# Kernel optimization log

Hardware: AMD Instinct MI355X
Metric: run time of the kernel (lower is better)

## Reference

```python
import jax, jax.numpy as jnp
import numpy as np
import math

B, S, D, NH = 2, 2048, 1024, 16
DK = D // NH
E, TOPK, MOE_H, NSH = 8, 2, 1024, 2
SH_H = MOE_H * NSH
EPS = 1e-6


def setup_inputs() -> dict:
    key = jax.random.key(0)
    ks = jax.random.split(key, 24)
    p = lambda k, shape: jax.random.normal(k, shape, jnp.float32) * 0.02
    x = jax.random.normal(ks[0], (B, S, D), jnp.float32)
    # RoPE tables: freqs_cis = exp(i * t * theta^{-2j/dk}), passed as cos/sin
    inv = 1.0 / (10000.0 ** (np.arange(0, DK, 2, dtype=np.float32) / DK))
    ang = np.outer(np.arange(S, dtype=np.float32), inv)
    freqs_cos = jnp.asarray(np.cos(ang), jnp.float32)
    freqs_sin = jnp.asarray(np.sin(ang), jnp.float32)
    mask = jnp.triu(jnp.full((S, S), -1e9, jnp.float32), k=1)  # causal additive mask
    return {
        'x': x, 'freqs_cos': freqs_cos, 'freqs_sin': freqs_sin, 'mask': mask,
        'wq': p(ks[1], (D, D)), 'wk': p(ks[2], (D, D)),
        'wv': p(ks[3], (D, D)), 'wo': p(ks[4], (D, D)),
        'attn_norm_w': jnp.ones((D,), jnp.float32),
        'ffn_norm_w': jnp.ones((D,), jnp.float32),
        'gate_w': p(ks[5], (E, D)), 'gate_b': p(ks[6], (E,)),
        'w1': p(ks[7], (E, MOE_H, D)), 'b1': p(ks[8], (E, MOE_H)),
        'w2': p(ks[9], (E, D, MOE_H)), 'b2': p(ks[10], (E, D)),
        'w3': p(ks[11], (E, MOE_H, D)), 'b3': p(ks[12], (E, MOE_H)),
        'sg_w': p(ks[13], (SH_H, D)), 'su_w': p(ks[14], (SH_H, D)),
        'sd_w': p(ks[15], (D, SH_H)),
    }


def rmsnorm(x, w):
    f = x.astype(jnp.float32)
    y = f * jax.lax.rsqrt(jnp.mean(f * f, axis=-1, keepdims=True) + EPS)
    return y.astype(x.dtype) * w


def rope(t, cos, sin):
    # t: [b, s, h, dk]; pairs (t[2j], t[2j+1]) as complex, multiplied by e^{i ang}
    tr, ti = t[..., 0::2], t[..., 1::2]
    c, s = cos[None, :, None, :], sin[None, :, None, :]
    outr = tr * c - ti * s
    outi = tr * s + ti * c
    return jnp.stack([outr, outi], axis=-1).reshape(t.shape)


def reference(x, freqs_cos, freqs_sin, mask, wq, wk, wv, wo, attn_norm_w, ffn_norm_w,
              gate_w, gate_b, w1, b1, w2, b2, w3, b3, sg_w, su_w, sd_w):
    b, s, d = x.shape
    # --- attention with RoPE ---
    h = rmsnorm(x, attn_norm_w)
    q = (h @ wq.T).reshape(b, s, NH, DK)
    k = (h @ wk.T).reshape(b, s, NH, DK)
    v = (h @ wv.T).reshape(b, s, NH, DK)
    q = rope(q, freqs_cos, freqs_sin)
    k = rope(k, freqs_cos, freqs_sin)
    scale = 1.0 / math.sqrt(DK)
    q = q.transpose(0, 2, 1, 3)
    k = k.transpose(0, 2, 1, 3)
    v = v.transpose(0, 2, 1, 3)
    scores = jnp.einsum('bhqd,bhkd->bhqk', q, k) * scale + mask
    # NOTE: source divides by sqrt(d_k) a second time before softmax (faithful quirk)
    attn = jax.nn.softmax(scores * scale, axis=-1)
    o = jnp.einsum('bhqk,bhkd->bhqd', attn, v).transpose(0, 2, 1, 3).reshape(b, s, d)
    x = x + o @ wo.T
    # --- MoE FFN ---
    hf = rmsnorm(x, ffn_norm_w).reshape(-1, d)                 # [T, D]
    gscores = jax.nn.softmax(hf @ gate_w.T + gate_b, axis=-1)  # [T, E]
    _, idx = jax.lax.top_k(gscores, TOPK)                      # bias is None -> topk on scores
    weights = jnp.take_along_axis(gscores, idx, axis=1)        # original_scores gather
    wmask = (jax.nn.one_hot(idx, E, dtype=hf.dtype) * weights[..., None]).sum(1)  # [T, E]
    shared = (jax.nn.silu(hf @ sg_w.T) * (hf @ su_w.T)) @ sd_w.T
    a1 = jnp.einsum('td,ehd->teh', hf, w1) + b1
    a3 = jnp.einsum('td,ehd->teh', hf, w3) + b3
    eo = jnp.einsum('teh,edh->ted', jax.nn.silu(a1) * a3, w2) + b2  # [T, E, D]
    router = jnp.einsum('te,ted->td', wmask, eo)
    return x + (shared + router).reshape(x.shape)
```

## Files before the change

### kernel.cpp

```cpp
#include <hip/hip_runtime.h>


typedef unsigned short u16;
typedef __attribute__((ext_vector_type(8))) short bh8;
typedef __attribute__((ext_vector_type(4))) float fv4;
typedef __attribute__((ext_vector_type(4))) unsigned uv4;
typedef __attribute__((ext_vector_type(2))) int iv2;

#define LOG2E 1.4426950408889634f
#define MAX_TILES 71

__device__ __forceinline__ float b2f(u16 u) {
  return __builtin_bit_cast(float, ((unsigned)u) << 16);
}
__device__ __forceinline__ u16 f2b(float f) {
  unsigned x = __builtin_bit_cast(unsigned, f);
  return (u16)((x + 0x7fffu + ((x >> 16) & 1u)) >> 16);
}
__device__ __forceinline__ fv4 mfma16(bh8 a, bh8 b, fv4 c) {
  return __builtin_amdgcn_mfma_f32_16x16x32_bf16(a, b, c, 0, 0, 0);
}
__device__ __forceinline__ unsigned cvtpk(float lo, float hi) {
  unsigned r;
  asm("v_cvt_pk_bf16_f32 %0, %1, %2" : "=v"(r) : "v"(lo), "v"(hi));
  return r;
}

__device__ __forceinline__ void xcd_swizzle(int& bx, int& by) {
  int gx = gridDim.x;
  int nwg = gx * gridDim.y;
  int flat = by * gx + bx;
  int q = nwg >> 3, r = nwg & 7;
  int xcd = flat & 7, idx = flat >> 3;
  int swz = (xcd < r ? xcd * (q + 1) : r * (q + 1) + (xcd - r) * q) + idx;
  by = swz / gx;
  bx = swz - by * gx;
}

#define GLD16(g, l)                                                        \
  __builtin_amdgcn_global_load_lds(                                        \
      (const __attribute__((address_space(1))) void*)(g),                  \
      (__attribute__((address_space(3))) void*)(l), 16, 0, 0)

__device__ __forceinline__ bh8 lds_frag(const u16* base, int row, int b8) {
  int off = row * 128 + ((b8 * 16) ^ ((row & 7) << 4));
  return *(const bh8*)((const char*)base + off);
}

template <int MODE, int TM = 128>
__global__ __launch_bounds__(256) void gemm_bt(
    const u16* __restrict__ A, const u16* __restrict__ B, int M, int N, int K,
    u16* __restrict__ Cb, float* __restrict__ Cf,
    const float* __restrict__ add1, const float* __restrict__ add2,
    const float* __restrict__ bias, const int* __restrict__ tmeta,
    const int* __restrict__ etok) {
  constexpr int MR = TM / 32;
  __shared__ u16 As[2][TM * 64];
  __shared__ u16 Bs[2][128 * 64];
  int bx = blockIdx.x, by = blockIdx.y;
  xcd_swizzle(bx, by);
  const int lane = threadIdx.x & 63;
  const int wid = threadIdx.x >> 6;
  const int wr = wid >> 1, wc = wid & 1;
  const int n0 = bx * 128;
  const int rr = lane >> 3;
  const int b8s = (lane & 7) ^ rr;
  const int ldA = (MODE == 6) ? M : K;

  int m0 = 0, e = 0, m0l = 0, cnt = 0, row0 = 0;
  const u16* Bp = B;
  if constexpr (MODE == 6 || MODE == 8) {
    int tile = by;
    if (tile >= tmeta[0]) return;
    e = tmeta[16 + tile * 4];
    m0l = tmeta[17 + tile * 4];
    cnt = tmeta[18 + tile * 4];
    row0 = tmeta[19 + tile * 4];
    Bp = B + (size_t)e * N * K;
  } else {
    m0 = by * TM;
  }

  const u16* Arow[MR];
  const u16* Brow[4];
#pragma unroll
  for (int i = 0; i < MR; ++i) {
    int c = wid * MR + i;
    int row = c * 8 + rr;
    if constexpr (MODE == 8) {
      int li = m0l + row;
      li = li < cnt ? li : cnt - 1;
      int tok = etok[e * 4096 + li];
      Arow[i] = A + (size_t)tok * ldA + b8s * 8;
    } else if constexpr (MODE == 6) {
      Arow[i] = A + (size_t)(row0 + row) * ldA + b8s * 8;
    } else {
      Arow[i] = A + (size_t)(m0 + row) * ldA + b8s * 8;
    }
  }
#pragma unroll
  for (int i = 0; i < 4; ++i)
    Brow[i] = Bp + (size_t)(n0 + (wid * 4 + i) * 8 + rr) * K + b8s * 8;

  fv4 acc[MR][4] = {};
  const int nt = K >> 6;

#pragma unroll
  for (int i = 0; i < MR; ++i)
    GLD16(Arow[i], &As[0][(wid * MR + i) * 512]);
#pragma unroll
  for (int i = 0; i < 4; ++i)
    GLD16(Brow[i], &Bs[0][(wid * 4 + i) * 512]);

  for (int t = 0; t < nt; ++t) {
    const int cur = t & 1;
    if (t + 1 < nt) {
      const int k0 = (t + 1) * 64;
#pragma unroll
      for (int i = 0; i < MR; ++i)
        GLD16(Arow[i] + k0, &As[cur ^ 1][(wid * MR + i) * 512]);
#pragma unroll
      for (int i = 0; i < 4; ++i)
        GLD16(Brow[i] + k0, &Bs[cur ^ 1][(wid * 4 + i) * 512]);
      if constexpr (MR == 4)
        asm volatile("s_waitcnt vmcnt(8)" ::: "memory");
      else
        asm volatile("s_waitcnt vmcnt(6)" ::: "memory");
    } else {
      asm volatile("s_waitcnt vmcnt(0)" ::: "memory");
    }
    __builtin_amdgcn_s_barrier();
    __builtin_amdgcn_sched_barrier(0);

#pragma unroll
    for (int ks = 0; ks < 2; ++ks) {
      int b8 = ks * 4 + (lane >> 4);
      bh8 af[MR], bf[4];
#pragma unroll
      for (int mi = 0; mi < MR; ++mi)
        af[mi] = lds_frag(As[cur], wr * (16 * MR) + mi * 16 + (lane & 15), b8);
#pragma unroll
      for (int ni = 0; ni < 4; ++ni)
        bf[ni] = lds_frag(Bs[cur], wc * 64 + ni * 16 + (lane & 15), b8);
      __builtin_amdgcn_s_setprio(1);
#pragma unroll
      for (int mi = 0; mi < MR; ++mi)
#pragma unroll
        for (int ni = 0; ni < 4; ++ni)
          acc[mi][ni] = mfma16(af[mi], bf[ni], acc[mi][ni]);
      __builtin_amdgcn_s_setprio(0);
    }
    __builtin_amdgcn_sched_barrier(0);
    __builtin_amdgcn_s_barrier();
    __builtin_amdgcn_sched_barrier(0);
  }

  const int rbase = (MODE == 6 || MODE == 8) ? row0 : m0;
  const int r0b = rbase + wr * (16 * MR) + (lane >> 4) * 4;
  const int c0b = n0 + wc * 64 + (lane & 15);

  if constexpr (MODE == 7 || MODE == 8) {
    const int OUTN = N >> 1;
    const int colb = (n0 >> 1) + wc * 32;
    const float* bb1 = nullptr;
    const float* bb3 = nullptr;
    if constexpr (MODE == 8) {
      bb1 = add1 + (size_t)e * OUTN;
      bb3 = add2 + (size_t)e * OUTN;
    }
#pragma unroll
    for (int mi = 0; mi < MR; ++mi) {
#pragma unroll
      for (int ni = 0; ni < 2; ++ni) {
        int c = colb + ni * 16 + (lane & 15);
#pragma unroll
        for (int r = 0; r < 4; ++r) {
          int row = r0b + mi * 16 + r;
          float xg = acc[mi][ni][r];
          float yu = acc[mi][ni + 2][r];
          if constexpr (MODE == 8) {
            xg += bb1[c];
            yu += bb3[c];
          }
          float s = xg / (1.f + __expf(-xg));
          Cb[(size_t)row * OUTN + c] = f2b(s * yu);
        }
      }
    }
  } else if constexpr (MODE == 9) {
#pragma unroll
    for (int mi = 0; mi < MR; ++mi) {
#pragma unroll
      for (int r = 0; r < 4; ++r) {
        int row = r0b + mi * 16 + r;
        int g0 = tmeta[2 * row], g1 = tmeta[2 * row + 1];
        float w0 = bias[2 * row], w1 = bias[2 * row + 1];
        const u16* e0p = Cb + (size_t)g0 * 1024;
        const u16* e1p = Cb + (size_t)g1 * 1024;
#pragma unroll
        for (int ni = 0; ni < 4; ++ni) {
          int c = c0b + ni * 16;
          size_t idx = (size_t)row * N + c;
          Cf[idx] = add1[idx] + acc[mi][ni][r] + w0 * b2f(e0p[c]) +
                    w1 * b2f(e1p[c]);
        }
      }
    }
  } else {
    const float* bb = nullptr;
    if constexpr (MODE == 6) bb = bias + (size_t)e * N;
#pragma unroll
    for (int mi = 0; mi < MR; ++mi) {
#pragma unroll
      for (int ni = 0; ni < 4; ++ni) {
        int c = c0b + ni * 16;
#pragma unroll
        for (int r = 0; r < 4; ++r) {
          int row = r0b + mi * 16 + r;
          size_t idx = (size_t)row * N + c;
          float v = acc[mi][ni][r];
          if constexpr (MODE == 0) Cb[idx] = f2b(v);
          else if constexpr (MODE == 1) Cf[idx] = add1[idx] + v;
          else Cb[idx] = f2b(v + bb[c]);
        }
      }
    }
  }
}

__global__ __launch_bounds__(256) void rmsnorm_bf16(
    const float* __restrict__ x, const float* __restrict__ w,
    u16* __restrict__ out) {
  int t = blockIdx.x;
  const float* xr = x + (size_t)t * 1024;
  fv4 v = *(const fv4*)(xr + threadIdx.x * 4);
  float ss = v[0] * v[0] + v[1] * v[1] + v[2] * v[2] + v[3] * v[3];
#pragma unroll
  for (int off = 1; off < 64; off <<= 1) ss += __shfl_xor(ss, off);
  __shared__ float red[4];
  int lane = threadIdx.x & 63, wid = threadIdx.x >> 6;
  if (lane == 0) red[wid] = ss;
  __syncthreads();
  float inv = rsqrtf((red[0] + red[1] + red[2] + red[3]) * (1.0f / 1024.f) + 1e-6f);
  u16* op = out + (size_t)t * 1024 + threadIdx.x * 4;
  const float* wp = w + threadIdx.x * 4;
#pragma unroll
  for (int i = 0; i < 4; ++i) op[i] = f2b(v[i] * inv * wp[i]);
}

__global__ __launch_bounds__(256) void rope_repack(
    const u16* __restrict__ qkv, const float* __restrict__ fc,
    const float* __restrict__ fs, u16* __restrict__ qr, u16* __restrict__ kr,
    u16* __restrict__ vt, int S) {
  __shared__ u16 tile[64][65];
  const int s0 = blockIdx.x * 64;
  const int b = blockIdx.y;
  const int h0 = blockIdx.z * 4;
#pragma unroll 4
  for (int it = 0; it < 32; ++it) {
    int idx = threadIdx.x + it * 256;
    int tl = idx >> 7, rem = idx & 127;
    int h = h0 + (rem >> 5), i = rem & 31;
    int s = s0 + tl;
    float c = fc[s * 32 + i], sn = fs[s * 32 + i];
    size_t src = ((size_t)(b * S + s)) * 3072 + h * 64 + 2 * i;
    size_t dst = ((size_t)((b * 16 + h) * S + s)) * 64 + 2 * i;
    float a0 = b2f(qkv[src]), a1 = b2f(qkv[src + 1]);
    qr[dst] = f2b(a0 * c - a1 * sn);
    qr[dst + 1] = f2b(a0 * sn + a1 * c);
    float b0 = b2f(qkv[src + 1024]), b1 = b2f(qkv[src + 1025]);
    kr[dst] = f2b(b0 * c - b1 * sn);
    kr[dst + 1] = f2b(b0 * sn + b1 * c);
  }
  for (int hh = 0; hh < 4; ++hh) {
    int h = h0 + hh;
    __syncthreads();
    for (int cc = threadIdx.x; cc < 512; cc += 256) {
      int tl = cc >> 3, d8 = cc & 7;
      bh8 val = *(const bh8*)(qkv + ((size_t)(b * S + s0 + tl)) * 3072 + 2048 +
                              h * 64 + d8 * 8);
#pragma unroll
      for (int j = 0; j < 8; ++j) tile[tl][d8 * 8 + j] = (u16)val[j];
    }
    __syncthreads();
    for (int cc = threadIdx.x; cc < 512; cc += 256) {
      int d = cc >> 3, pg = cc & 7;
      int sbase = 16 * (pg >> 2) + 4 * (pg & 3);
      bh8 o;
#pragma unroll
      for (int j = 0; j < 8; ++j)
        o[j] = (short)tile[sbase + (j & 3) + ((j >> 2) << 5)][d];
      *(bh8*)(vt + ((size_t)((b * 16 + h) * 64 + d)) * S + s0 + pg * 8) = o;
    }
  }
}

__global__ __launch_bounds__(256) void attn_fwd(
    const u16* __restrict__ qr, const u16* __restrict__ kr,
    const u16* __restrict__ vt, u16* __restrict__ ob, int S, int NHc) {
  __shared__ u16 Ks[2][64 * 64];
  __shared__ u16 Vs[2][64 * 64];
  const int lane = threadIdx.x & 63;
  const int wid = threadIdx.x >> 6;
  const int g = lane >> 4;
  const int l15 = lane & 15;
  const int bh = blockIdx.x;
  const int ia = blockIdx.y;
  const int nq = S / 64;
  const int qa0 = ia * 64;
  const int qb0 = (nq - 1 - ia) * 64;
  const int b = bh / NHc, h = bh % NHc;
  const u16* qbase = qr + (size_t)bh * S * 64;
  const u16* kb = kr + (size_t)bh * S * 64;
  const u16* vb = vt + (size_t)bh * 64 * S;
  const float SC = 0.015625f * LOG2E;
  const int rr = lane >> 3;
  const int b8s = (lane & 7) ^ rr;

  bh8 ONES;
#pragma unroll
  for (int j = 0; j < 8; ++j) ONES[j] = (short)0x3f80;

  bh8 qfA[2], qfB[2];
  {
    const u16* qp = qbase + (size_t)(qa0 + wid * 16 + l15) * 64 + g * 8;
    qfA[0] = *(const bh8*)qp;
    qfA[1] = *(const bh8*)(qp + 32);
    qp = qbase + (size_t)(qb0 + wid * 16 + l15) * 64 + g * 8;
    qfB[0] = *(const bh8*)qp;
    qfB[1] = *(const bh8*)(qp + 32);
  }
  fv4 oaccA[4] = {}, oaccB[4] = {};
  fv4 lA = {}, lB = {};
  float mA = -1e30f, mB = -1e30f;
  const int nktB = nq - ia;

  auto stage = [&](int buf, int j0) {
#pragma unroll
    for (int i = 0; i < 2; ++i) {
      int c = wid * 2 + i;
      int row = c * 8 + rr;
      GLD16(kb + (size_t)(j0 + row) * 64 + b8s * 8, &Ks[buf][c * 512]);
      GLD16(vb + (size_t)row * S + j0 + b8s * 8, &Vs[buf][c * 512]);
    }
  };
  stage(0, 0);

  auto process = [&](const bh8 (&kf)[2][4], const bh8 (&vf)[2][4], int j0,
                     int q0x, bh8* qf, fv4* oacc, float& mrow, fv4& lrowC) {
    const int q_my = q0x + wid * 16 + l15;
    fv4 st[4] = {};
    __builtin_amdgcn_s_setprio(1);
#pragma unroll
    for (int ks = 0; ks < 2; ++ks)
#pragma unroll
      for (int jt = 0; jt < 4; ++jt)
        st[jt] = mfma16(kf[ks][jt], qf[ks], st[jt]);
    __builtin_amdgcn_s_setprio(0);

    float sr[4][4];
    float mloc = -1e30f;
    const int jb = j0 + 4 * g;
    if (j0 + 63 > q0x + wid * 16) {
#pragma unroll
      for (int jt = 0; jt < 4; ++jt)
#pragma unroll
        for (int r = 0; r < 4; ++r) {
          int j = jb + jt * 16 + r;
          float s = (j <= q_my) ? st[jt][r] : -1e30f;
          sr[jt][r] = s;
          mloc = fmaxf(mloc, s);
        }
    } else {
#pragma unroll
      for (int jt = 0; jt < 4; ++jt)
#pragma unroll
        for (int r = 0; r < 4; ++r) {
          sr[jt][r] = st[jt][r];
          mloc = fmaxf(mloc, st[jt][r]);
        }
    }
    mloc = fmaxf(mloc, __shfl_xor(mloc, 16));
    mloc = fmaxf(mloc, __shfl_xor(mloc, 32));
    mloc *= SC;
    bool defer = __all(mloc <= mrow + 8.f);
    if (!defer) {
      float mnew = fmaxf(mrow, mloc);
      float sfac = exp2f(mrow - mnew);
      mrow = mnew;
      float sfC[4];
#pragma unroll
      for (int r = 0; r < 4; ++r) sfC[r] = __shfl(sfac, g * 4 + r);
#pragma unroll
      for (int dt = 0; dt < 4; ++dt)
#pragma unroll
        for (int r = 0; r < 4; ++r) oacc[dt][r] *= sfC[r];
#pragma unroll
      for (int r = 0; r < 4; ++r) lrowC[r] *= sfC[r];
    }
    float p[4][4];
#pragma unroll
    for (int jt = 0; jt < 4; ++jt)
#pragma unroll
      for (int r = 0; r < 4; ++r)
        p[jt][r] = exp2f(fmaf(sr[jt][r], SC, -mrow));

    __builtin_amdgcn_s_setprio(1);
    fv4 racc = {};
#pragma unroll
    for (int ks = 0; ks < 2; ++ks) {
      uv4 w;
      w[0] = cvtpk(p[ks][0], p[ks][1]);
      w[1] = cvtpk(p[ks][2], p[ks][3]);
      w[2] = cvtpk(p[ks + 2][0], p[ks + 2][1]);
      w[3] = cvtpk(p[ks + 2][2], p[ks + 2][3]);
      bh8 pa = __builtin_bit_cast(bh8, w);
      racc = mfma16(pa, ONES, racc);
#pragma unroll
      for (int dt = 0; dt < 4; ++dt)
        oacc[dt] = mfma16(pa, vf[ks][dt], oacc[dt]);
    }
    __builtin_amdgcn_s_setprio(0);
#pragma unroll
    for (int r = 0; r < 4; ++r) lrowC[r] += racc[r];
  };

  for (int kt = 0; kt < nktB; ++kt) {
    const int j0 = kt * 64;
    __syncthreads();
    if (kt + 1 < nktB) stage((kt + 1) & 1, (kt + 1) * 64);
    const u16* Kc = Ks[kt & 1];
    const u16* Vc = Vs[kt & 1];
    bh8 kf[2][4], vf[2][4];
#pragma unroll
    for (int ks = 0; ks < 2; ++ks) {
      int b8 = ks * 4 + g;
#pragma unroll
      for (int jt = 0; jt < 4; ++jt)
        kf[ks][jt] = lds_frag(Kc, jt * 16 + l15, b8);
#pragma unroll
      for (int dt = 0; dt < 4; ++dt)
        vf[ks][dt] = lds_frag(Vc, dt * 16 + l15, b8);
    }
    process(kf, vf, j0, qb0, qfB, oaccB, mB, lB);
    if (kt <= ia) process(kf, vf, j0, qa0, qfA, oaccA, mA, lA);
  }

  auto wout = [&](fv4* oacc, fv4 lrowC, int q0x) {
#pragma unroll
    for (int dt = 0; dt < 4; ++dt)
#pragma unroll
      for (int r = 0; r < 4; ++r) {
        int row = q0x + wid * 16 + g * 4 + r;
        int col = dt * 16 + l15;
        ob[((size_t)b * S + row) * 1024 + h * 64 + col] =
            f2b(oacc[dt][r] / lrowC[r]);
      }
  };
  wout(oaccA, lA, qa0);
  wout(oaccB, lB, qb0);
}

__global__ __launch_bounds__(256) void gate_topk(
    const float* __restrict__ x2, const float* __restrict__ nw,
    const float* __restrict__ gw, const float* __restrict__ gb,
    int* __restrict__ topk_e, float* __restrict__ topk_w,
    u16* __restrict__ hf) {
  int t = blockIdx.x * 4 + (threadIdx.x >> 6);
  int lane = threadIdx.x & 63;
  const float* xr = x2 + (size_t)t * 1024;
  float hv[16];
  float ss = 0.f;
#pragma unroll
  for (int i = 0; i < 4; ++i) {
    fv4 v = *(const fv4*)(xr + lane * 16 + i * 4);
#pragma unroll
    for (int j = 0; j < 4; ++j) {
      hv[i * 4 + j] = v[j];
      ss += v[j] * v[j];
    }
  }
#pragma unroll
  for (int off = 1; off < 64; off <<= 1) ss += __shfl_xor(ss, off);
  float inv = rsqrtf(ss * (1.0f / 1024.f) + 1e-6f);
  const fv4* nwp = (const fv4*)(nw + lane * 16);
#pragma unroll
  for (int i = 0; i < 4; ++i) {
    fv4 wv = nwp[i];
#pragma unroll
    for (int j = 0; j < 4; ++j) hv[i * 4 + j] *= inv * wv[j];
  }
  {
    bh8 o0, o1;
#pragma unroll
    for (int j = 0; j < 8; ++j) {
      o0[j] = (short)f2b(hv[j]);
      o1[j] = (short)f2b(hv[8 + j]);
    }
    u16* hp = hf + (size_t)t * 1024 + lane * 16;
    *(bh8*)hp = o0;
    *(bh8*)(hp + 8) = o1;
  }
  float logit[8];
#pragma unroll
  for (int e = 0; e < 8; ++e) {
    const fv4* wp = (const fv4*)(gw + (size_t)e * 1024 + lane * 16);
    float s = 0.f;
#pragma unroll
    for (int i = 0; i < 4; ++i) {
      fv4 wv = wp[i];
#pragma unroll
      for (int j = 0; j < 4; ++j) s += hv[i * 4 + j] * wv[j];
    }
    logit[e] = s;
  }
#pragma unroll
  for (int off = 1; off < 64; off <<= 1)
#pragma unroll
    for (int e = 0; e < 8; ++e) logit[e] += __shfl_xor(logit[e], off);
  if (lane == 0) {
#pragma unroll
    for (int e = 0; e < 8; ++e) logit[e] += gb[e];
    float mx = logit[0];
#pragma unroll
    for (int e = 1; e < 8; ++e) mx = fmaxf(mx, logit[e]);
    float pe[8], se = 0.f;
#pragma unroll
    for (int e = 0; e < 8; ++e) { pe[e] = __expf(logit[e] - mx); se += pe[e]; }
    float rs = 1.f / se;
#pragma unroll
    for (int e = 0; e < 8; ++e) pe[e] *= rs;
    int i0 = 0;
    float b0 = pe[0];
#pragma unroll
    for (int e = 1; e < 8; ++e)
      if (pe[e] > b0) { b0 = pe[e]; i0 = e; }
    int i1 = -1;
    float b1v = -1.f;
#pragma unroll
    for (int e = 0; e < 8; ++e)
      if (e != i0 && pe[e] > b1v) { b1v = pe[e]; i1 = e; }
    topk_e[2 * t] = i0;
    topk_e[2 * t + 1] = i1;
    topk_w[2 * t] = b0;
    topk_w[2 * t + 1] = b1v;
  }
}

__global__ __launch_bounds__(512) void route_tokens(
    const int* __restrict__ topk_e, int* __restrict__ pos_of,
    int* __restrict__ etok, int* __restrict__ meta, int* __restrict__ rowid,
    int T2) {
  __shared__ int scnt[8], sbase[8];
  const int e = threadIdx.x >> 6;
  const int lane = threadIdx.x & 63;
  int base = 0;
  for (int i0 = 0; i0 < T2; i0 += 128) {
    iv2 te = *(const iv2*)(topk_e + i0 + lane * 2);
    unsigned long long m0 = __ballot(te[0] == e);
    unsigned long long m1 = __ballot(te[1] == e);
    unsigned long long lt = (1ull << lane) - 1;
    int pre = __popcll(m0 & lt) + __popcll(m1 & lt);
    if (te[0] == e) {
      int pos = base + pre;
      etok[e * 4096 + pos] = (i0 >> 1) + lane;
      pos_of[i0 + lane * 2] = pos;
      ++pre;
    }
    if (te[1] == e) {
      int pos = base + pre;
      etok[e * 4096 + pos] = (i0 >> 1) + lane;
      pos_of[i0 + lane * 2 + 1] = pos;
    }
    base += __popcll(m0) + __popcll(m1);
  }
  if (lane == 0) scnt[e] = base;
  __syncthreads();
  if (threadIdx.x == 0) {
    int tt = 0, rb = 0;
#pragma unroll
    for (int e2 = 0; e2 < 8; ++e2) {
      sbase[e2] = rb;
      int c = scnt[e2];
      int nt = (c + 127) >> 7;
      for (int i = 0; i < nt; ++i) {
        meta[16 + tt * 4] = e2;
        meta[17 + tt * 4] = i * 128;
        meta[18 + tt * 4] = c;
        meta[19 + tt * 4] = rb + i * 128;
        ++tt;
      }
      rb += nt * 128;
    }
    meta[0] = tt;
  }
  __syncthreads();
  for (int i = threadIdx.x; i < T2; i += 512)
    rowid[i] = sbase[topk_e[i]] + pos_of[i];
}

__global__ __launch_bounds__(256) void f2b_convert(
    const float* __restrict__ src, u16* __restrict__ dst) {
  size_t i = ((size_t)blockIdx.x * 256 + threadIdx.x) * 8;
  fv4 a = *(const fv4*)(src + i);
  fv4 b = *(const fv4*)(src + i + 4);
  bh8 o;
#pragma unroll
  for (int j = 0; j < 4; ++j) o[j] = (short)f2b(a[j]);
#pragma unroll
  for (int j = 0; j < 4; ++j) o[4 + j] = (short)f2b(b[j]);
  *(bh8*)(dst + i) = o;
}

__global__ __launch_bounds__(256) void f2b_convert_ilv(
    const float* __restrict__ src, u16* __restrict__ dst, int half,
    int seg_shift) {
  size_t i = ((size_t)blockIdx.x * 256 + threadIdx.x) * 8;
  int r = (int)(i >> 10), col = (int)(i & 1023);
  int rl = r & ((1 << seg_shift) - 1), e = r >> seg_shift;
  int dstrow = (e << (seg_shift + 1)) + ((rl >> 5) << 6) + (rl & 31) +
               (half << 5);
  fv4 a = *(const fv4*)(src + i);
  fv4 b = *(const fv4*)(src + i + 4);
  bh8 o;
#pragma unroll
  for (int j = 0; j < 4; ++j) o[j] = (short)f2b(a[j]);
#pragma unroll
  for (int j = 0; j < 4; ++j) o[4 + j] = (short)f2b(b[j]);
  *(bh8*)(dst + (size_t)dstrow * 1024 + col) = o;
}

extern "C" void kernel_launch(void* const* d_in, const int* in_sizes, int n_in,
                              void* d_out, int out_size, void* d_ws,
                              size_t ws_size, hipStream_t stream) {
  (void)in_sizes; (void)n_in; (void)out_size; (void)ws_size;
  const int Sc = 2048, Dc = 1024, NHc = 16, Tc = 4096, SH = 2048;

  const float* x   = (const float*)d_in[0];
  const float* fc  = (const float*)d_in[1];
  const float* fs  = (const float*)d_in[2];
  const float* wq  = (const float*)d_in[4];
  const float* wk  = (const float*)d_in[5];
  const float* wv  = (const float*)d_in[6];
  const float* wo  = (const float*)d_in[7];
  const float* anw = (const float*)d_in[8];
  const float* fnw = (const float*)d_in[9];
  const float* gw  = (const float*)d_in[10];
  const float* gb  = (const float*)d_in[11];
  const float* w1  = (const float*)d_in[12];
  const float* b1  = (const float*)d_in[13];
  const float* w2  = (const float*)d_in[14];
  const float* b2  = (const float*)d_in[15];
  const float* w3  = (const float*)d_in[16];
  const float* b3  = (const float*)d_in[17];
  const float* sgw = (const float*)d_in[18];
  const float* suw = (const float*)d_in[19];
  const float* sdw = (const float*)d_in[20];
  float* out = (float*)d_out;

  char* base = (char*)d_ws;
  size_t off = 0;
  auto alloc = [&](size_t bytes) -> void* {
    void* p = base + off;
    off += (bytes + 255) & ~(size_t)255;
    return p;
  };
  u16* wqkv_b = (u16*)alloc(2ull * 3072 * 1024);
  u16* wo_b   = (u16*)alloc(2ull * 1024 * 1024);
  u16* sgu_b  = (u16*)alloc(2ull * 4096 * 1024);
  u16* sdw_b  = (u16*)alloc(2ull * 1024 * 2048);
  u16* w13_b  = (u16*)alloc(2ull * 8 * 2048 * 1024);
  u16* w2_b   = (u16*)alloc(2ull * 8 * 1024 * 1024);
  char* regA = (char*)alloc(2ull * Tc * 4096);
  char* regB = (char*)alloc(2ull * (size_t)MAX_TILES * 128 * 2048);
  float* x2  = (float*)alloc(4ull * Tc * Dc);
  u16* hs_b  = (u16*)alloc(2ull * Tc * SH);
  int* topk_e = (int*)alloc(2ull * Tc * 4);
  float* topk_w = (float*)alloc(2ull * Tc * 4);
  int* pos_of = (int*)alloc(2ull * Tc * 4);
  int* rowid = (int*)alloc(2ull * Tc * 4);
  int* etok = (int*)alloc(8ull * 4096 * 4);
  int* meta = (int*)alloc(512 * 4);

  u16* qkv_out = (u16*)regA;
  u16* eo_c    = (u16*)regA;
  u16* h_b  = (u16*)regB;
  u16* qr   = (u16*)regB;
  u16* kr   = (u16*)(regB + 2ull * Tc * Dc);
  u16* vt_  = (u16*)(regB + 4ull * Tc * Dc);
  u16* o_b  = (u16*)(regB + 6ull * Tc * Dc);
  u16* a13_c = (u16*)regB;
  u16* hf_b = wqkv_b;

  auto conv = [&](const float* s, u16* d, size_t n) {
    f2b_convert<<<dim3((unsigned)(n / 2048)), 256, 0, stream>>>(s, d);
  };
  conv(wq, wqkv_b, (size_t)Dc * Dc);
  conv(wk, wqkv_b + 1048576, (size_t)Dc * Dc);
  conv(wv, wqkv_b + 2097152, (size_t)Dc * Dc);
  conv(wo, wo_b, (size_t)Dc * Dc);
  conv(sdw, sdw_b, (size_t)Dc * SH);
  conv(w2, w2_b, 8ull * 1024 * 1024);
  f2b_convert_ilv<<<1024, 256, 0, stream>>>(sgw, sgu_b, 0, 11);
  f2b_convert_ilv<<<1024, 256, 0, stream>>>(suw, sgu_b, 1, 11);
  f2b_convert_ilv<<<4096, 256, 0, stream>>>(w1, w13_b, 0, 10);
  f2b_convert_ilv<<<4096, 256, 0, stream>>>(w3, w13_b, 1, 10);

  rmsnorm_bf16<<<Tc, 256, 0, stream>>>(x, anw, h_b);
  gemm_bt<0><<<dim3(3072 / 128, Tc / 128), 256, 0, stream>>>(
      h_b, wqkv_b, Tc, 3072, Dc, qkv_out, nullptr, nullptr, nullptr, nullptr,
      nullptr, nullptr);
  rope_repack<<<dim3(Sc / 64, 2, 4), 256, 0, stream>>>(qkv_out, fc, fs, qr, kr,
                                                       vt_, Sc);
  attn_fwd<<<dim3(2 * NHc, Sc / 128), 256, 0, stream>>>(qr, kr, vt_, o_b, Sc,
                                                        NHc);
  gemm_bt<1, 64><<<dim3(Dc / 128, Tc / 64), 256, 0, stream>>>(
      o_b, wo_b, Tc, Dc, Dc, nullptr, x2, x, nullptr, nullptr, nullptr,
      nullptr);

  gate_topk<<<Tc / 4, 256, 0, stream>>>(x2, fnw, gw, gb, topk_e, topk_w,
                                        hf_b);
  route_tokens<<<1, 512, 0, stream>>>(topk_e, pos_of, etok, meta, rowid,
                                      2 * Tc);

  gemm_bt<7><<<dim3(4096 / 128, Tc / 128), 256, 0, stream>>>(
      hf_b, sgu_b, Tc, 4096, Dc, hs_b, nullptr, nullptr, nullptr, nullptr,
      nullptr, nullptr);

  gemm_bt<8><<<dim3(2048 / 128, MAX_TILES), 256, 0, stream>>>(
      hf_b, w13_b, Tc, 2048, Dc, a13_c, nullptr, b1, b3, nullptr, meta, etok);
  gemm_bt<6><<<dim3(Dc / 128, MAX_TILES), 256, 0, stream>>>(
      a13_c, w2_b, 1024, Dc, 1024, eo_c, nullptr, nullptr, nullptr,
      b2, meta, etok);

  gemm_bt<9, 64><<<dim3(Dc / 128, Tc / 64), 256, 0, stream>>>(
      hs_b, sdw_b, Tc, Dc, SH, eo_c, out, x2, nullptr, topk_w, rowid,
      nullptr);
}
```

Baseline: 406.6 us.

## Use 4-stage BK=32 LDS pipeline in gemm_bt instead of double-buffered BK=64

Restructures the GEMM main loop from a two-buffer pipeline with 64-wide K tiles into a four-buffer ring with 32-wide K tiles. Loads run three stages ahead, with waitcnt values graded for the tail. It adds a new 32-column LDS swizzle (lds_frag32) and remaps global-to-LDS loads to match. The goal is to hide global load latency behind more in-flight stages at the same LDS footprint. The cost is twice as many barriers per unit of K and fewer MFMAs between barriers.

Result: slower. 446.4 us (+9.8%).

```diff
diff --git a/kernel.cpp b/kernel.cpp
--- a/kernel.cpp
+++ b/kernel.cpp
@@ -42,6 +42,11 @@
       (const __attribute__((address_space(1))) void*)(g),                  \
       (__attribute__((address_space(3))) void*)(l), 16, 0, 0)
 
+__device__ __forceinline__ bh8 lds_frag32(const u16* base, int row, int g) {
+  int off = (row << 5) + (((g ^ (row >> 1)) & 3) << 3);
+  return *(const bh8*)(base + off);
+}
+
 __device__ __forceinline__ bh8 lds_frag(const u16* base, int row, int b8) {
   int off = row * 128 + ((b8 * 16) ^ ((row & 7) << 4));
   return *(const bh8*)((const char*)base + off);
@@ -55,16 +60,19 @@
     const float* __restrict__ bias, const int* __restrict__ tmeta,
     const int* __restrict__ etok) {
   constexpr int MR = TM / 32;
-  __shared__ u16 As[2][TM * 64];
-  __shared__ u16 Bs[2][128 * 64];
+  constexpr int AC = MR / 2;
+  __shared__ u16 As[4][TM * 32];
+  __shared__ u16 Bs[4][128 * 32];
   int bx = blockIdx.x, by = blockIdx.y;
   xcd_swizzle(bx, by);
   const int lane = threadIdx.x & 63;
   const int wid = threadIdx.x >> 6;
   const int wr = wid >> 1, wc = wid & 1;
   const int n0 = bx * 128;
-  const int rr = lane >> 3;
-  const int b8s = (lane & 7) ^ rr;
+  const int l15 = lane & 15;
+  const int g4 = lane >> 4;
+  const int rr = lane >> 2;
+  const int usrc = (lane & 3) ^ ((rr >> 1) & 3);
   const int ldA = (MODE == 6) ? M : K;
 
   int m0 = 0, e = 0, m0l = 0, cnt = 0, row0 = 0;
@@ -81,75 +89,82 @@
     m0 = by * TM;
   }
 
-  const u16* Arow[MR];
-  const u16* Brow[4];
-#pragma unroll
-  for (int i = 0; i < MR; ++i) {
-    int c = wid * MR + i;
-    int row = c * 8 + rr;
+  const u16* ArowP[AC];
+  const u16* BrowP[2];
+#pragma unroll
+  for (int i = 0; i < AC; ++i) {
+    int row = (wid * AC + i) * 16 + rr;
     if constexpr (MODE == 8) {
       int li = m0l + row;
       li = li < cnt ? li : cnt - 1;
       int tok = etok[e * 4096 + li];
-      Arow[i] = A + (size_t)tok * ldA + b8s * 8;
+      ArowP[i] = A + (size_t)tok * ldA + usrc * 8;
     } else if constexpr (MODE == 6) {
-      Arow[i] = A + (size_t)(row0 + row) * ldA + b8s * 8;
+      ArowP[i] = A + (size_t)(row0 + row) * ldA + usrc * 8;
     } else {
-      Arow[i] = A + (size_t)(m0 + row) * ldA + b8s * 8;
-    }
-  }
-#pragma unroll
-  for (int i = 0; i < 4; ++i)
-    Brow[i] = Bp + (size_t)(n0 + (wid * 4 + i) * 8 + rr) * K + b8s * 8;
+      ArowP[i] = A + (size_t)(m0 + row) * ldA + usrc * 8;
+    }
+  }
+#pragma unroll
+  for (int i = 0; i < 2; ++i)
+    BrowP[i] = Bp + (size_t)(n0 + (wid * 2 + i) * 16 + rr) * K + usrc * 8;
 
   fv4 acc[MR][4] = {};
-  const int nt = K >> 6;
-
-#pragma unroll
-  for (int i = 0; i < MR; ++i)
-    GLD16(Arow[i], &As[0][(wid * MR + i) * 512]);
-#pragma unroll
-  for (int i = 0; i < 4; ++i)
-    GLD16(Brow[i], &Bs[0][(wid * 4 + i) * 512]);
+  const int nt = K >> 5;
+
+  auto stage = [&](int tt) {
+    const int buf = tt & 3;
+    const int k0 = tt << 5;
+#pragma unroll
+    for (int i = 0; i < AC; ++i)
+      GLD16(ArowP[i] + k0, &As[buf][(wid * AC + i) * 512]);
+#pragma unroll
+    for (int i = 0; i < 2; ++i)
+      GLD16(BrowP[i] + k0, &Bs[buf][(wid * 2 + i) * 512]);
+  };
+  stage(0);
+  stage(1);
+  stage(2);
 
   for (int t = 0; t < nt; ++t) {
-    const int cur = t & 1;
-    if (t + 1 < nt) {
-      const int k0 = (t + 1) * 64;
-#pragma unroll
-      for (int i = 0; i < MR; ++i)
-        GLD16(Arow[i] + k0, &As[cur ^ 1][(wid * MR + i) * 512]);
-#pragma unroll
-      for (int i = 0; i < 4; ++i)
-        GLD16(Brow[i] + k0, &Bs[cur ^ 1][(wid * 4 + i) * 512]);
+    const int cur = t & 3;
+    if (t + 3 < nt) stage(t + 3);
+    __builtin_amdgcn_sched_barrier(0);
+    if (t + 3 < nt) {
+      if constexpr (MR == 4)
+        asm volatile("s_waitcnt vmcnt(12)" ::: "memory");
+      else
+        asm volatile("s_waitcnt vmcnt(9)" ::: "memory");
+    } else if (t + 2 < nt) {
       if constexpr (MR == 4)
         asm volatile("s_waitcnt vmcnt(8)" ::: "memory");
       else
         asm volatile("s_waitcnt vmcnt(6)" ::: "memory");
+    } else if (t + 1 < nt) {
+      if constexpr (MR == 4)
+        asm volatile("s_waitcnt vmcnt(4)" ::: "memory");
+      else
+        asm volatile("s_waitcnt vmcnt(3)" ::: "memory");
     } else {
       asm volatile("s_waitcnt vmcnt(0)" ::: "memory");
     }
     __builtin_amdgcn_s_barrier();
     __builtin_amdgcn_sched_barrier(0);
 
-#pragma unroll
-    for (int ks = 0; ks < 2; ++ks) {
-      int b8 = ks * 4 + (lane >> 4);
-      bh8 af[MR], bf[4];
-#pragma unroll
-      for (int mi = 0; mi < MR; ++mi)
-        af[mi] = lds_frag(As[cur], wr * (16 * MR) + mi * 16 + (lane & 15), b8);
+    bh8 af[MR], bf[4];
+#pragma unroll
+    for (int mi = 0; mi < MR; ++mi)
+      af[mi] = lds_frag32(As[cur], wr * (16 * MR) + mi * 16 + l15, g4);
+#pragma unroll
+    for (int ni = 0; ni < 4; ++ni)
+      bf[ni] = lds_frag32(Bs[cur], wc * 64 + ni * 16 + l15, g4);
+    __builtin_amdgcn_s_setprio(1);
+#pragma unroll
+    for (int mi = 0; mi < MR; ++mi)
 #pragma unroll
       for (int ni = 0; ni < 4; ++ni)
-        bf[ni] = lds_frag(Bs[cur], wc * 64 + ni * 16 + (lane & 15), b8);
-      __builtin_amdgcn_s_setprio(1);
-#pragma unroll
-      for (int mi = 0; mi < MR; ++mi)
-#pragma unroll
-        for (int ni = 0; ni < 4; ++ni)
-          acc[mi][ni] = mfma16(af[mi], bf[ni], acc[mi][ni]);
-      __builtin_amdgcn_s_setprio(0);
-    }
+        acc[mi][ni] = mfma16(af[mi], bf[ni], acc[mi][ni]);
+    __builtin_amdgcn_s_setprio(0);
     __builtin_amdgcn_sched_barrier(0);
     __builtin_amdgcn_s_barrier();
     __builtin_amdgcn_sched_barrier(0);
```

## Merge shared-expert and routed-expert up GEMMs into one launch; halve w2 tile height

Applied to the files above, without the earlier changes.

The shared-expert gate/up GEMM and the routed-expert w1/w3 GEMM now run as one grouped kernel over a flattened, XCD-swizzled block index, with each block dispatching to the matching body. This removes a launch boundary and lets the two independent GEMMs fill the GPU together, so the tail of one overlaps the other. The expert down-projection GEMM now uses 64-row tiles, each 128-row tile split into two halves. That doubles the block count for the ragged expert workload and improves occupancy and load balance, at the cost of more B-operand reloads per block.

Measured after the change: 398.2 us. -2.1%, faster.

```diff
diff --git a/kernel.cpp b/kernel.cpp
--- a/kernel.cpp
+++ b/kernel.cpp
@@ -36,6 +36,11 @@
   by = swz / gx;
   bx = swz - by * gx;
 }
+__device__ __forceinline__ int xcd_swizzle1d(int flat, int nwg) {
+  int q = nwg >> 3, r = nwg & 7;
+  int xcd = flat & 7, idx = flat >> 3;
+  return (xcd < r ? xcd * (q + 1) : r * (q + 1) + (xcd - r) * q) + idx;
+}
 
 #define GLD16(g, l)                                                        \
   __builtin_amdgcn_global_load_lds(                                        \
@@ -47,18 +52,14 @@
   return *(const bh8*)((const char*)base + off);
 }
 
-template <int MODE, int TM = 128>
-__global__ __launch_bounds__(256) void gemm_bt(
-    const u16* __restrict__ A, const u16* __restrict__ B, int M, int N, int K,
-    u16* __restrict__ Cb, float* __restrict__ Cf,
-    const float* __restrict__ add1, const float* __restrict__ add2,
-    const float* __restrict__ bias, const int* __restrict__ tmeta,
-    const int* __restrict__ etok) {
+template <int MODE, int TM>
+__device__ __forceinline__ void gemm_body(
+    u16* AsB, u16* BsB, int bx, int by, const u16* __restrict__ A,
+    const u16* __restrict__ B, int M, int N, int K, u16* __restrict__ Cb,
+    float* __restrict__ Cf, const float* __restrict__ add1,
+    const float* __restrict__ add2, const float* __restrict__ bias,
+    const int* __restrict__ tmeta, const int* __restrict__ etok) {
   constexpr int MR = TM / 32;
-  __shared__ u16 As[2][TM * 64];
-  __shared__ u16 Bs[2][128 * 64];
-  int bx = blockIdx.x, by = blockIdx.y;
-  xcd_swizzle(bx, by);
   const int lane = threadIdx.x & 63;
   const int wid = threadIdx.x >> 6;
   const int wr = wid >> 1, wc = wid & 1;
@@ -70,12 +71,16 @@
   int m0 = 0, e = 0, m0l = 0, cnt = 0, row0 = 0;
   const u16* Bp = B;
   if constexpr (MODE == 6 || MODE == 8) {
-    int tile = by;
+    int tile = by, half = 0;
+    if constexpr (MODE == 6 && TM == 64) {
+      tile = by >> 1;
+      half = by & 1;
+    }
     if (tile >= tmeta[0]) return;
     e = tmeta[16 + tile * 4];
     m0l = tmeta[17 + tile * 4];
     cnt = tmeta[18 + tile * 4];
-    row0 = tmeta[19 + tile * 4];
+    row0 = tmeta[19 + tile * 4] + half * 64;
     Bp = B + (size_t)e * N * K;
   } else {
     m0 = by * TM;
@@ -107,21 +112,25 @@
 
 #pragma unroll
   for (int i = 0; i < MR; ++i)
-    GLD16(Arow[i], &As[0][(wid * MR + i) * 512]);
+    GLD16(Arow[i], &AsB[(wid * MR + i) * 512]);
 #pragma unroll
   for (int i = 0; i < 4; ++i)
-    GLD16(Brow[i], &Bs[0][(wid * 4 + i) * 512]);
+    GLD16(Brow[i], &BsB[(wid * 4 + i) * 512]);
 
   for (int t = 0; t < nt; ++t) {
     const int cur = t & 1;
+    u16* Asc = AsB + cur * (TM * 64);
+    u16* Bsc = BsB + cur * (128 * 64);
     if (t + 1 < nt) {
       const int k0 = (t + 1) * 64;
+      u16* Asn = AsB + (cur ^ 1) * (TM * 64);
+      u16* Bsn = BsB + (cur ^ 1) * (128 * 64);
 #pragma unroll
       for (int i = 0; i < MR; ++i)
-        GLD16(Arow[i] + k0, &As[cur ^ 1][(wid * MR + i) * 512]);
+        GLD16(Arow[i] + k0, &Asn[(wid * MR + i) * 512]);
 #pragma unroll
       for (int i = 0; i < 4; ++i)
-        GLD16(Brow[i] + k0, &Bs[cur ^ 1][(wid * 4 + i) * 512]);
+        GLD16(Brow[i] + k0, &Bsn[(wid * 4 + i) * 512]);
       if constexpr (MR == 4)
         asm volatile("s_waitcnt vmcnt(8)" ::: "memory");
       else
@@ -138,10 +147,10 @@
       bh8 af[MR], bf[4];
 #pragma unroll
       for (int mi = 0; mi < MR; ++mi)
-        af[mi] = lds_frag(As[cur], wr * (16 * MR) + mi * 16 + (lane & 15), b8);
+        af[mi] = lds_frag(Asc, wr * (16 * MR) + mi * 16 + (lane & 15), b8);
 #pragma unroll
       for (int ni = 0; ni < 4; ++ni)
-        bf[ni] = lds_frag(Bs[cur], wc * 64 + ni * 16 + (lane & 15), b8);
+        bf[ni] = lds_frag(Bsc, wc * 64 + ni * 16 + (lane & 15), b8);
       __builtin_amdgcn_s_setprio(1);
 #pragma unroll
       for (int mi = 0; mi < MR; ++mi)
@@ -225,6 +234,44 @@
         }
       }
     }
+  }
+}
+
+template <int MODE, int TM = 128>
+__global__ __launch_bounds__(256) void gemm_bt(
+    const u16* __restrict__ A, const u16* __restrict__ B, int M, int N, int K,
+    u16* __restrict__ Cb, float* __restrict__ Cf,
+    const float* __restrict__ add1, const float* __restrict__ add2,
+    const float* __restrict__ bias, const int* __restrict__ tmeta,
+    const int* __restrict__ etok) {
+  __shared__ u16 As[2][TM * 64];
+  __shared__ u16 Bs[2][128 * 64];
+  int bx = blockIdx.x, by = blockIdx.y;
+  xcd_swizzle(bx, by);
+  gemm_body<MODE, TM>(&As[0][0], &Bs[0][0], bx, by, A, B, M, N, K, Cb, Cf,
+                      add1, add2, bias, tmeta, etok);
+}
+
+__global__ __launch_bounds__(256) void gemm_sgu_w13(
+    const u16* __restrict__ hf, const u16* __restrict__ sgu_w,
+    u16* __restrict__ hs, const u16* __restrict__ w13_w,
+    u16* __restrict__ a13, const float* __restrict__ b1,
+    const float* __restrict__ b3, const int* __restrict__ meta,
+    const int* __restrict__ etok) {
+  __shared__ u16 As[2][128 * 64];
+  __shared__ u16 Bs[2][128 * 64];
+  const int nwg = 1024 + 16 * MAX_TILES;
+  int flat = xcd_swizzle1d((int)blockIdx.x, nwg);
+  if (flat < 1024) {
+    int by = flat >> 5, bx = flat & 31;
+    gemm_body<7, 128>(&As[0][0], &Bs[0][0], bx, by, hf, sgu_w, 4096, 4096,
+                      1024, hs, nullptr, nullptr, nullptr, nullptr, nullptr,
+                      nullptr);
+  } else {
+    int idx = flat - 1024;
+    int by = idx >> 4, bx = idx & 15;
+    gemm_body<8, 128>(&As[0][0], &Bs[0][0], bx, by, hf, w13_w, 4096, 2048,
+                      1024, a13, nullptr, b1, b3, nullptr, meta, etok);
   }
 }
 
@@ -723,13 +770,10 @@
   route_tokens<<<1, 512, 0, stream>>>(topk_e, pos_of, etok, meta, rowid,
                                       2 * Tc);
 
-  gemm_bt<7><<<dim3(4096 / 128, Tc / 128), 256, 0, stream>>>(
-      hf_b, sgu_b, Tc, 4096, Dc, hs_b, nullptr, nullptr, nullptr, nullptr,
-      nullptr, nullptr);
-
-  gemm_bt<8><<<dim3(2048 / 128, MAX_TILES), 256, 0, stream>>>(
-      hf_b, w13_b, Tc, 2048, Dc, a13_c, nullptr, b1, b3, nullptr, meta, etok);
-  gemm_bt<6><<<dim3(Dc / 128, MAX_TILES), 256, 0, stream>>>(
+  gemm_sgu_w13<<<dim3(1024 + 16 * MAX_TILES), 256, 0, stream>>>(
+      hf_b, sgu_b, hs_b, w13_b, a13_c, b1, b3, meta, etok);
+
+  gemm_bt<6, 64><<<dim3(Dc / 128, 2 * MAX_TILES), 256, 0, stream>>>(
       a13_c, w2_b, 1024, Dc, 1024, eo_c, nullptr, nullptr, nullptr,
       b2, meta, etok);
 
```
